# Optimization experiments

Measured on AMD Instinct MI355X. Metric: run time of the kernel, lower is better.

Reference implementation:

```python
import jax, jax.numpy as jnp
import numpy as np

B, L, S = 32, 8192, 128  # E == S == D == 128 required by the einsum labeling

def setup_inputs() -> dict:
    key = jax.random.key(0)
    kq, kk, kv = jax.random.split(key, 3)
    queries = jax.random.normal(kq, (B, L, S), dtype=jnp.float32)
    keys = jax.random.normal(kk, (B, S, S), dtype=jnp.float32)
    values = jax.random.normal(kv, (B, S, S), dtype=jnp.float32)
    return {"queries": queries, "keys": keys, "values": values}

def reference(queries, keys, values):
    # queries: (B, L, E), keys/values: (B, S, D) with E == S == D.
    # scores_1: sum-pooled outer product term (reduced-rank additive score)
    s1 = queries.sum(-1)[:, :, None] * keys.sum(-1)[:, None, :]   # (B, L, S)
    # scores_2: q contracted against key-position axis (plain batched matmul, no transpose)
    s2 = jnp.einsum('bls,bsd->bld', queries, keys)                # (B, L, S)
    A = jax.nn.softmax(s1 + s2, axis=-1)                          # (B, L, S)
    out = jnp.einsum('bls,bsd->bld', A, values)                   # (B, L, D)
    # original returns shape (B, 1, L, D) for the 3D-input path
    return out[:, None, :, :]
```

## Files before the change

kernel.cpp:

```cpp
#include <hip/hip_runtime.h>

#define SDIM 128
#define LDIM 8192
#define BATCH 32

#define WS_KSUM_BYTES 16384
#define WS_BATCH_BYTES 98304

typedef __attribute__((ext_vector_type(8))) short short8;
typedef __attribute__((ext_vector_type(16))) float float16;

static __device__ __forceinline__ unsigned short f2bf(float x) {
    union { float f; unsigned u; } v; v.f = x;
    unsigned r = v.u + 0x7fffu + ((v.u >> 16) & 1u);
    return (unsigned short)(r >> 16);
}
static __device__ __forceinline__ float bf2f(unsigned short h) {
    union { unsigned u; float f; } v; v.u = ((unsigned)h) << 16; return v.f;
}

union S8U { short8 v; unsigned short u[8]; unsigned w[4]; };

static __device__ __forceinline__ float16 mfma_bf16(short8 a, short8 b, float16 c) {
    return __builtin_amdgcn_mfma_f32_32x32x16_bf16(a, b, c, 0, 0, 0);
}

__global__ void ksum_kernel(const float* __restrict__ keys, float* __restrict__ ksum) {
    int gwave = (blockIdx.x * blockDim.x + threadIdx.x) >> 6;
    int lane = threadIdx.x & 63;
    const float* row = keys + (size_t)gwave * SDIM;
    float v = row[lane] + row[lane + 64];
    #pragma unroll
    for (int off = 32; off > 0; off >>= 1) v += __shfl_xor(v, off, 64);
    if (lane == 0) ksum[gwave] = v;
}

__global__ __launch_bounds__(256) void prep_kernel(
        const float* __restrict__ keys, const float* __restrict__ values,
        const float* __restrict__ ksum, char* __restrict__ ws) {
    __shared__ float T[SDIM * SDIM];
    const int b = blockIdx.x >> 1;
    const int which = blockIdx.x & 1;
    const int tid = threadIdx.x;
    const float* src = (which ? values : keys) + (size_t)b * SDIM * SDIM;

    for (int i = tid; i < SDIM * SDIM / 4; i += 256) {
        int r = i >> 5;
        int c0 = (i & 31) * 4;
        float4 v = ((const float4*)src)[i];
        float f[4] = {v.x, v.y, v.z, v.w};
        #pragma unroll
        for (int k = 0; k < 4; ++k)
            T[r * SDIM + ((c0 + k + r) & 127)] = f[k];
    }
    __syncthreads();

    char* dst = ws + WS_KSUM_BYTES + (size_t)b * WS_BATCH_BYTES + (which ? 65536 : 0);
    const float* ksb = ksum + b * SDIM;

    if (which == 0) {
        for (int idx = tid; idx < 2048; idx += 256) {
            int j = idx >> 4, c = idx & 15;
            float ks = ksb[j];
            S8U hi, lo;
            #pragma unroll
            for (int i2 = 0; i2 < 8; ++i2) {
                int e = c * 8 + i2;
                float x = T[e * SDIM + ((j + e) & 127)] + ks;
                unsigned short h = f2bf(x);
                hi.u[i2] = h;
                lo.u[i2] = f2bf(x - bf2f(h));
            }
            int off = j * 256 + ((c ^ (j & 15)) * 16);
            *(short8*)(dst + off) = hi.v;
            *(short8*)(dst + 32768 + off) = lo.v;
        }
    } else {
        for (int idx = tid; idx < 2048; idx += 256) {
            int d = idx >> 4, c = idx & 15;
            S8U hv;
            #pragma unroll
            for (int i2 = 0; i2 < 8; ++i2) {
                int j = c * 8 + i2;
                hv.u[i2] = f2bf(T[j * SDIM + ((d + j) & 127)]);
            }
            int off = d * 256 + ((c ^ (d & 15)) * 16);
            *(short8*)(dst + off) = hv.v;
        }
    }
}

__global__ __launch_bounds__(256, 2) void attn_kernel(
        const float* __restrict__ q, const char* __restrict__ ws,
        float* __restrict__ out) {
    __shared__ uint4 smem[4096];
    const int blk = blockIdx.x;
    const int b = blk >> 6;
    const int tile = blk & 63;
    const int tid = threadIdx.x;
    const int wave = tid >> 6;
    const int lane = tid & 63;
    const int H = lane >> 5;
    const int ln = lane & 31;

    const char* wsb = ws + WS_KSUM_BYTES + (size_t)b * WS_BATCH_BYTES;
    const float* qb = q + ((size_t)b * LDIM + tile * 128 + wave * 32) * SDIM;
    float* ob = out + ((size_t)b * LDIM + tile * 128 + wave * 32) * SDIM;

    {
        const uint4* s4 = (const uint4*)wsb;
        for (int i = tid; i < 4096; i += 256) smem[i] = s4[i];
    }
    __syncthreads();
    const char* sm = (const char*)smem;

    float16 acc[4];
    #pragma unroll
    for (int m = 0; m < 4; ++m) acc[m] = (float16)(0.0f);

    #pragma unroll
    for (int ks = 0; ks < 8; ++ks) {
        const float* qp = qb + ln * SDIM + ks * 16 + H * 8;
        float4 f0 = *(const float4*)qp;
        float4 f1 = *(const float4*)(qp + 4);
        float f[8] = {f0.x, f0.y, f0.z, f0.w, f1.x, f1.y, f1.z, f1.w};
        S8U bh, bl;
        #pragma unroll
        for (int i = 0; i < 8; ++i) {
            unsigned short h = f2bf(f[i]);
            bh.u[i] = h;
            bl.u[i] = f2bf(f[i] - bf2f(h));
        }
        const int chunk = ((2 * ks + H) ^ (lane & 15)) * 16;
        #pragma unroll
        for (int m = 0; m < 4; ++m) {
            int roff = (m * 32 + ln) * 256 + chunk;
            short8 ah = *(const short8*)(sm + roff);
            short8 al = *(const short8*)(sm + 32768 + roff);
            acc[m] = mfma_bf16(ah, bh.v, acc[m]);
            acc[m] = mfma_bf16(ah, bl.v, acc[m]);
            acc[m] = mfma_bf16(al, bh.v, acc[m]);
        }
    }

    float mx = -1e30f;
    #pragma unroll
    for (int m = 0; m < 4; ++m)
        #pragma unroll
        for (int r = 0; r < 16; ++r) mx = fmaxf(mx, acc[m][r]);
    mx = fmaxf(mx, __shfl_xor(mx, 32, 64));
    float sum = 0.0f;
    #pragma unroll
    for (int m = 0; m < 4; ++m)
        #pragma unroll
        for (int r = 0; r < 16; ++r) {
            float e = __expf(acc[m][r] - mx);
            acc[m][r] = e;
            sum += e;
        }
    sum += __shfl_xor(sum, 32, 64);
    const float inv = 1.0f / sum;

    unsigned pk[4][8];
    #pragma unroll
    for (int m = 0; m < 4; ++m)
        #pragma unroll
        for (int rr = 0; rr < 8; ++rr)
            pk[m][rr] = (unsigned)f2bf(acc[m][2 * rr] * inv) |
                        ((unsigned)f2bf(acc[m][2 * rr + 1] * inv) << 16);

    __syncthreads();
    {
        const uint4* s4 = (const uint4*)(wsb + 65536);
        for (int i = tid; i < 2048; i += 256) smem[i] = s4[i];
    }
    __syncthreads();

    float16 oacc[4];
    #pragma unroll
    for (int m = 0; m < 4; ++m) oacc[m] = (float16)(0.0f);

    #pragma unroll
    for (int t = 0; t < 8; ++t) {
        const int m = t >> 1;
        const int c = 4 * (t & 1);
        unsigned p0 = pk[m][c], p1 = pk[m][c + 1], p2 = pk[m][c + 2], p3 = pk[m][c + 3];
        unsigned a0 = H ? p2 : p0, a1 = H ? p3 : p1;
        unsigned s0 = H ? p0 : p2, s1 = H ? p1 : p3;
        unsigned r0 = (unsigned)__shfl_xor((int)s0, 32, 64);
        unsigned r1 = (unsigned)__shfl_xor((int)s1, 32, 64);
        S8U bf;
        bf.w[0] = H ? r0 : a0;
        bf.w[1] = H ? r1 : a1;
        bf.w[2] = H ? a0 : r0;
        bf.w[3] = H ? a1 : r1;
        const int chunk = ((2 * t + H) ^ (lane & 15)) * 16;
        #pragma unroll
        for (int dm = 0; dm < 4; ++dm) {
            short8 af = *(const short8*)(sm + (dm * 32 + ln) * 256 + chunk);
            oacc[dm] = mfma_bf16(af, bf.v, oacc[dm]);
        }
    }

    #pragma unroll
    for (int dm = 0; dm < 4; ++dm)
        #pragma unroll
        for (int g = 0; g < 4; ++g) {
            float4 v = make_float4(oacc[dm][4 * g], oacc[dm][4 * g + 1],
                                   oacc[dm][4 * g + 2], oacc[dm][4 * g + 3]);
            int d0 = dm * 32 + g * 8 + H * 4;
            *(float4*)(ob + ln * SDIM + d0) = v;
        }
}

extern "C" void kernel_launch(void* const* d_in, const int* in_sizes, int n_in,
                              void* d_out, int out_size, void* d_ws, size_t ws_size,
                              hipStream_t stream) {
    const float* q    = (const float*)d_in[0];
    const float* keys = (const float*)d_in[1];
    const float* vals = (const float*)d_in[2];
    float* out  = (float*)d_out;
    float* ksum = (float*)d_ws;
    char*  ws   = (char*)d_ws;

    ksum_kernel<<<(BATCH * SDIM * 64) / 256, 256, 0, stream>>>(keys, ksum);
    prep_kernel<<<BATCH * 2, 256, 0, stream>>>(keys, vals, ksum, ws);
    attn_kernel<<<BATCH * (LDIM / 128), 256, 0, stream>>>(q, ws, out);
}
```

Baseline: 275.6 us.

## Pre-arrange K/V in MFMA fragment order, stage Q in LDS, fuse ksum into prep

```diff
diff --git a/kernel.cpp b/kernel.cpp
--- a/kernel.cpp
+++ b/kernel.cpp
@@ -4,49 +4,42 @@
 #define LDIM 8192
 #define BATCH 32
 
-#define WS_KSUM_BYTES 16384
 #define WS_BATCH_BYTES 98304
 
 typedef __attribute__((ext_vector_type(8))) short short8;
 typedef __attribute__((ext_vector_type(16))) float float16;
 
+union S8U { short8 v; unsigned short u[8]; unsigned w[4]; };
+union FU { float f; unsigned u; };
+
 static __device__ __forceinline__ unsigned short f2bf(float x) {
-    union { float f; unsigned u; } v; v.f = x;
+    FU v; v.f = x;
     unsigned r = v.u + 0x7fffu + ((v.u >> 16) & 1u);
     return (unsigned short)(r >> 16);
 }
 static __device__ __forceinline__ float bf2f(unsigned short h) {
-    union { unsigned u; float f; } v; v.u = ((unsigned)h) << 16; return v.f;
-}
-
-union S8U { short8 v; unsigned short u[8]; unsigned w[4]; };
-
+    FU v; v.u = ((unsigned)h) << 16; return v.f;
+}
 static __device__ __forceinline__ float16 mfma_bf16(short8 a, short8 b, float16 c) {
     return __builtin_amdgcn_mfma_f32_32x32x16_bf16(a, b, c, 0, 0, 0);
 }
 
-__global__ void ksum_kernel(const float* __restrict__ keys, float* __restrict__ ksum) {
-    int gwave = (blockIdx.x * blockDim.x + threadIdx.x) >> 6;
-    int lane = threadIdx.x & 63;
-    const float* row = keys + (size_t)gwave * SDIM;
-    float v = row[lane] + row[lane + 64];
-    #pragma unroll
-    for (int off = 32; off > 0; off >>= 1) v += __shfl_xor(v, off, 64);
-    if (lane == 0) ksum[gwave] = v;
-}
-
 __global__ __launch_bounds__(256) void prep_kernel(
         const float* __restrict__ keys, const float* __restrict__ values,
-        const float* __restrict__ ksum, char* __restrict__ ws) {
+        char* __restrict__ ws) {
     __shared__ float T[SDIM * SDIM];
-    const int b = blockIdx.x >> 1;
-    const int which = blockIdx.x & 1;
+    __shared__ float ksum_s[SDIM];
+    const int blk = blockIdx.x;
+    const int b = blk >> 2;
+    const int which = (blk >> 1) & 1;
+    const int half = blk & 1;
     const int tid = threadIdx.x;
     const float* src = (which ? values : keys) + (size_t)b * SDIM * SDIM;
 
-    for (int i = tid; i < SDIM * SDIM / 4; i += 256) {
-        int r = i >> 5;
-        int c0 = (i & 31) * 4;
+    #pragma unroll
+    for (int it = 0; it < 16; ++it) {
+        int i = tid + it * 256;
+        int r = i >> 5, c0 = (i & 31) * 4;
         float4 v = ((const float4*)src)[i];
         float f[4] = {v.x, v.y, v.z, v.w};
         #pragma unroll
@@ -55,37 +48,47 @@
     }
     __syncthreads();
 
-    char* dst = ws + WS_KSUM_BYTES + (size_t)b * WS_BATCH_BYTES + (which ? 65536 : 0);
-    const float* ksb = ksum + b * SDIM;
-
     if (which == 0) {
-        for (int idx = tid; idx < 2048; idx += 256) {
-            int j = idx >> 4, c = idx & 15;
-            float ks = ksb[j];
+        int row = tid >> 1, hf = tid & 1;
+        float s = 0.f;
+        #pragma unroll
+        for (int i = 0; i < 64; ++i) s += T[row * SDIM + hf * 64 + i];
+        s += __shfl_xor(s, 1, 64);
+        if (hf == 0) ksum_s[row] = s;
+    }
+    __syncthreads();
+
+    char* dst = ws + (size_t)b * WS_BATCH_BYTES + (which ? 65536 : 0);
+    #pragma unroll
+    for (int it = 0; it < 4; ++it) {
+        int entry = half * 1024 + it * 256 + tid;
+        int m = entry >> 9;
+        int ks = (entry >> 6) & 7;
+        int lane = entry & 63;
+        int ln = lane & 31, H = lane >> 5;
+        int r = 32 * m + ln;
+        int c0 = 16 * ks + 8 * H;
+        if (which == 0) {
+            float add = ksum_s[r];
             S8U hi, lo;
             #pragma unroll
-            for (int i2 = 0; i2 < 8; ++i2) {
-                int e = c * 8 + i2;
-                float x = T[e * SDIM + ((j + e) & 127)] + ks;
+            for (int i = 0; i < 8; ++i) {
+                int e = c0 + i;
+                float x = T[e * SDIM + ((r + e) & 127)] + add;
                 unsigned short h = f2bf(x);
-                hi.u[i2] = h;
-                lo.u[i2] = f2bf(x - bf2f(h));
-            }
-            int off = j * 256 + ((c ^ (j & 15)) * 16);
-            *(short8*)(dst + off) = hi.v;
-            *(short8*)(dst + 32768 + off) = lo.v;
-        }
-    } else {
-        for (int idx = tid; idx < 2048; idx += 256) {
-            int d = idx >> 4, c = idx & 15;
+                hi.u[i] = h;
+                lo.u[i] = f2bf(x - bf2f(h));
+            }
+            *(short8*)(dst + entry * 16) = hi.v;
+            *(short8*)(dst + 32768 + entry * 16) = lo.v;
+        } else {
             S8U hv;
             #pragma unroll
-            for (int i2 = 0; i2 < 8; ++i2) {
-                int j = c * 8 + i2;
-                hv.u[i2] = f2bf(T[j * SDIM + ((d + j) & 127)]);
-            }
-            int off = d * 256 + ((c ^ (d & 15)) * 16);
-            *(short8*)(dst + off) = hv.v;
+            for (int i = 0; i < 8; ++i) {
+                int j = c0 + i;
+                hv.u[i] = f2bf(T[j * SDIM + ((r + j) & 127)]);
+            }
+            *(short8*)(dst + entry * 16) = hv.v;
         }
     }
 }
@@ -93,55 +96,90 @@
 __global__ __launch_bounds__(256, 2) void attn_kernel(
         const float* __restrict__ q, const char* __restrict__ ws,
         float* __restrict__ out) {
-    __shared__ uint4 smem[4096];
+    __shared__ char smQ[65536];
     const int blk = blockIdx.x;
-    const int b = blk >> 6;
-    const int tile = blk & 63;
-    const int tid = threadIdx.x;
-    const int wave = tid >> 6;
-    const int lane = tid & 63;
-    const int H = lane >> 5;
-    const int ln = lane & 31;
-
-    const char* wsb = ws + WS_KSUM_BYTES + (size_t)b * WS_BATCH_BYTES;
-    const float* qb = q + ((size_t)b * LDIM + tile * 128 + wave * 32) * SDIM;
+    const int b = blk >> 6, tile = blk & 63;
+    const int tid = threadIdx.x, wave = tid >> 6, lane = tid & 63;
+    const int H = lane >> 5, ln = lane & 31;
+
+    const char* wsb = ws + (size_t)b * WS_BATCH_BYTES;
+    const float* qblk = q + ((size_t)b * LDIM + tile * 128) * SDIM;
     float* ob = out + ((size_t)b * LDIM + tile * 128 + wave * 32) * SDIM;
 
     {
-        const uint4* s4 = (const uint4*)wsb;
-        for (int i = tid; i < 4096; i += 256) smem[i] = s4[i];
+        float4 buf[8][2];
+        #pragma unroll
+        for (int it = 0; it < 8; ++it) {
+            int idx = it * 256 + tid;
+            const float* p = qblk + (idx >> 4) * SDIM + (idx & 15) * 8;
+            buf[it][0] = *(const float4*)p;
+            buf[it][1] = *(const float4*)(p + 4);
+        }
+        #pragma unroll
+        for (int it = 0; it < 8; ++it) {
+            int idx = it * 256 + tid;
+            int row = idx >> 4, cc = idx & 15;
+            float f[8] = {buf[it][0].x, buf[it][0].y, buf[it][0].z, buf[it][0].w,
+                          buf[it][1].x, buf[it][1].y, buf[it][1].z, buf[it][1].w};
+            unsigned hiw[4], low[4];
+            #pragma unroll
+            for (int pr = 0; pr < 4; ++pr) {
+                FU u0, u1; u0.f = f[2 * pr]; u1.f = f[2 * pr + 1];
+                unsigned r0 = u0.u + 0x7fffu + ((u0.u >> 16) & 1u);
+                unsigned r1 = u1.u + 0x7fffu + ((u1.u >> 16) & 1u);
+                hiw[pr] = (r0 >> 16) | (r1 & 0xffff0000u);
+                FU h0, h1; h0.u = r0 & 0xffff0000u; h1.u = r1 & 0xffff0000u;
+                FU l0, l1; l0.f = f[2 * pr] - h0.f; l1.f = f[2 * pr + 1] - h1.f;
+                low[pr] = (l0.u >> 16) | (l1.u & 0xffff0000u);
+            }
+            int off = row * 256 + ((cc ^ (row & 15)) * 16);
+            *(uint4*)(smQ + off) = make_uint4(hiw[0], hiw[1], hiw[2], hiw[3]);
+            *(uint4*)(smQ + 32768 + off) = make_uint4(low[0], low[1], low[2], low[3]);
+        }
     }
     __syncthreads();
-    const char* sm = (const char*)smem;
+
+    const char* qrp = smQ + (wave * 32 + ln) * 256;
+    const char* kph = wsb;
+    const char* kpl = wsb + 32768;
+    const char* vtf = wsb + 65536;
+    const int lo16 = lane * 16;
 
     float16 acc[4];
     #pragma unroll
     for (int m = 0; m < 4; ++m) acc[m] = (float16)(0.0f);
 
+    short8 ah[2][4], al[2][4];
+    #pragma unroll
+    for (int m = 0; m < 4; ++m) {
+        ah[0][m] = *(const short8*)(kph + (m * 8) * 1024 + lo16);
+        al[0][m] = *(const short8*)(kpl + (m * 8) * 1024 + lo16);
+    }
     #pragma unroll
     for (int ks = 0; ks < 8; ++ks) {
-        const float* qp = qb + ln * SDIM + ks * 16 + H * 8;
-        float4 f0 = *(const float4*)qp;
-        float4 f1 = *(const float4*)(qp + 4);
-        float f[8] = {f0.x, f0.y, f0.z, f0.w, f1.x, f1.y, f1.z, f1.w};
-        S8U bh, bl;
-        #pragma unroll
-        for (int i = 0; i < 8; ++i) {
-            unsigned short h = f2bf(f[i]);
-            bh.u[i] = h;
-            bl.u[i] = f2bf(f[i] - bf2f(h));
-        }
-        const int chunk = ((2 * ks + H) ^ (lane & 15)) * 16;
-        #pragma unroll
-        for (int m = 0; m < 4; ++m) {
-            int roff = (m * 32 + ln) * 256 + chunk;
-            short8 ah = *(const short8*)(sm + roff);
-            short8 al = *(const short8*)(sm + 32768 + roff);
-            acc[m] = mfma_bf16(ah, bh.v, acc[m]);
-            acc[m] = mfma_bf16(ah, bl.v, acc[m]);
-            acc[m] = mfma_bf16(al, bh.v, acc[m]);
-        }
-    }
+        const int cur = ks & 1, nxt = cur ^ 1;
+        if (ks < 7) {
+            #pragma unroll
+            for (int m = 0; m < 4; ++m) {
+                ah[nxt][m] = *(const short8*)(kph + (m * 8 + ks + 1) * 1024 + lo16);
+                al[nxt][m] = *(const short8*)(kpl + (m * 8 + ks + 1) * 1024 + lo16);
+            }
+        }
+        int slot = ((2 * ks + H) ^ (ln & 15)) * 16;
+        short8 bh = *(const short8*)(qrp + slot);
+        short8 bl = *(const short8*)(qrp + 32768 + slot);
+        #pragma unroll
+        for (int m = 0; m < 4; ++m) acc[m] = mfma_bf16(ah[cur][m], bh, acc[m]);
+        #pragma unroll
+        for (int m = 0; m < 4; ++m) acc[m] = mfma_bf16(ah[cur][m], bl, acc[m]);
+        #pragma unroll
+        for (int m = 0; m < 4; ++m) acc[m] = mfma_bf16(al[cur][m], bh, acc[m]);
+    }
+
+    short8 av[2][4];
+    #pragma unroll
+    for (int dm = 0; dm < 4; ++dm)
+        av[0][dm] = *(const short8*)(vtf + (dm * 8) * 1024 + lo16);
 
     float mx = -1e30f;
     #pragma unroll
@@ -169,19 +207,18 @@
             pk[m][rr] = (unsigned)f2bf(acc[m][2 * rr] * inv) |
                         ((unsigned)f2bf(acc[m][2 * rr + 1] * inv) << 16);
 
-    __syncthreads();
-    {
-        const uint4* s4 = (const uint4*)(wsb + 65536);
-        for (int i = tid; i < 2048; i += 256) smem[i] = s4[i];
-    }
-    __syncthreads();
-
     float16 oacc[4];
     #pragma unroll
     for (int m = 0; m < 4; ++m) oacc[m] = (float16)(0.0f);
 
     #pragma unroll
     for (int t = 0; t < 8; ++t) {
+        const int cur = t & 1, nxt = cur ^ 1;
+        if (t < 7) {
+            #pragma unroll
+            for (int dm = 0; dm < 4; ++dm)
+                av[nxt][dm] = *(const short8*)(vtf + (dm * 8 + t + 1) * 1024 + lo16);
+        }
         const int m = t >> 1;
         const int c = 4 * (t & 1);
         unsigned p0 = pk[m][c], p1 = pk[m][c + 1], p2 = pk[m][c + 2], p3 = pk[m][c + 3];
@@ -194,12 +231,9 @@
         bf.w[1] = H ? r1 : a1;
         bf.w[2] = H ? a0 : r0;
         bf.w[3] = H ? a1 : r1;
-        const int chunk = ((2 * t + H) ^ (lane & 15)) * 16;
-        #pragma unroll
-        for (int dm = 0; dm < 4; ++dm) {
-            short8 af = *(const short8*)(sm + (dm * 32 + ln) * 256 + chunk);
-            oacc[dm] = mfma_bf16(af, bf.v, oacc[dm]);
-        }
+        #pragma unroll
+        for (int dm = 0; dm < 4; ++dm)
+            oacc[dm] = mfma_bf16(av[cur][dm], bf.v, oacc[dm]);
     }
 
     #pragma unroll
@@ -208,8 +242,7 @@
         for (int g = 0; g < 4; ++g) {
             float4 v = make_float4(oacc[dm][4 * g], oacc[dm][4 * g + 1],
                                    oacc[dm][4 * g + 2], oacc[dm][4 * g + 3]);
-            int d0 = dm * 32 + g * 8 + H * 4;
-            *(float4*)(ob + ln * SDIM + d0) = v;
+            *(float4*)(ob + ln * SDIM + dm * 32 + g * 8 + H * 4) = v;
         }
 }
 
@@ -219,11 +252,9 @@
     const float* q    = (const float*)d_in[0];
     const float* keys = (const float*)d_in[1];
     const float* vals = (const float*)d_in[2];
-    float* out  = (float*)d_out;
-    float* ksum = (float*)d_ws;
-    char*  ws   = (char*)d_ws;
-
-    ksum_kernel<<<(BATCH * SDIM * 64) / 256, 256, 0, stream>>>(keys, ksum);
-    prep_kernel<<<BATCH * 2, 256, 0, stream>>>(keys, vals, ksum, ws);
+    float* out = (float*)d_out;
+    char*  ws  = (char*)d_ws;
+
+    prep_kernel<<<BATCH * 4, 256, 0, stream>>>(keys, vals, ws);
     attn_kernel<<<BATCH * (LDIM / 128), 256, 0, stream>>>(q, ws, out);
 }
```

After: 275.1 us. Within noise of the previous version (-0.2%).
